# Kernel optimization log

Measured on AMD Instinct MI355X. Metric: run time of the kernel, lower is better.

The kernel has to match this reference:

```python
import jax, jax.numpy as jnp
import numpy as np

EPS_MASK = 1e-9   # module fills masked scores with eps, NOT -inf
LN_EPS = 1e-5

def _layer_norm(x, g, b):
    mu = jnp.mean(x, axis=-1, keepdims=True)
    var = jnp.mean(jnp.square(x - mu), axis=-1, keepdims=True)
    return (x - mu) * jax.lax.rsqrt(var + LN_EPS) * g + b

def _mha(q_in, k_in, v_in, wq, bq, wk, bk, wv, bv, wo, bo, mask, nhead):
    B, Sq, D = q_in.shape
    dk = D // nhead
    def proj(x, w, b):
        y = x @ w + b                                   # [B,S,D]
        return y.reshape(B, -1, nhead, dk).transpose(0, 2, 1, 3)  # [B,h,S,dk]
    q, k, v = proj(q_in, wq, bq), proj(k_in, wk, bk), proj(v_in, wv, bv)
    scores = jnp.einsum('bhqd,bhkd->bhqk', q, k) / np.sqrt(dk).astype(q.dtype)
    if mask is not None:
        scores = jnp.where(mask[:, None, :, :] == 0, jnp.asarray(EPS_MASK, scores.dtype), scores)
    p = jax.nn.softmax(scores, axis=-1)                 # dropout = identity (eval)
    x = jnp.einsum('bhqk,bhkd->bhqd', p, v)
    x = x.transpose(0, 2, 1, 3).reshape(B, Sq, D)
    return x @ wo + bo

def _forward_post(tgt, memory, tgt_pos, memory_pos, tgt_mask, memory_mask, p):
    nhead = 8
    # self-attention (q=k=tgt+pos, v=tgt)
    q = tgt + tgt_pos
    sa = _mha(q, q, tgt, p['sa_wq'], p['sa_bq'], p['sa_wk'], p['sa_bk'],
              p['sa_wv'], p['sa_bv'], p['sa_wo'], p['sa_bo'], tgt_mask, nhead)
    tgt = _layer_norm(tgt + sa, p['ln1_g'], p['ln1_b'])
    # cross-attention (q=tgt+tgt_pos, k=memory+memory_pos, v=memory)
    mq = tgt + tgt_pos
    mk = memory + memory_pos
    ca = _mha(mq, mk, memory, p['ca_wq'], p['ca_bq'], p['ca_wk'], p['ca_bk'],
              p['ca_wv'], p['ca_bv'], p['ca_wo'], p['ca_bo'], memory_mask, nhead)
    tgt = _layer_norm(tgt + ca, p['ln2_g'], p['ln2_b'])
    # FFN
    h = jax.nn.relu(tgt @ p['mlp_w1'] + p['mlp_b1'])
    ff = h @ p['mlp_w2'] + p['mlp_b2']
    return _layer_norm(tgt + ff, p['ln3_g'], p['ln3_b'])

def setup_inputs() -> dict:
    key = jax.random.key(0)
    B, S, M, D, H = 4, 1024, 1024, 512, 2048
    ks = iter(jax.random.split(key, 40))
    d = {
        'tgt': jax.random.normal(next(ks), (B, S, D), jnp.float32),
        'memory': jax.random.normal(next(ks), (B, M, D), jnp.float32),
        'tgt_pos': jax.random.normal(next(ks), (B, S, D), jnp.float32),
        'memory_pos': jax.random.normal(next(ks), (B, M, D), jnp.float32),
        'tgt_mask': jax.random.randint(next(ks), (B, S, S), 0, 2, jnp.int32),
        'memory_mask': jax.random.randint(next(ks), (B, S, M), 0, 2, jnp.int32),
    }
    for pre in ('sa', 'ca'):
        for nm in ('q', 'k', 'v', 'o'):
            d[f'{pre}_w{nm}'] = jax.random.normal(next(ks), (D, D), jnp.float32) * 0.02
            d[f'{pre}_b{nm}'] = jnp.zeros((D,), jnp.float32)
    for i in (1, 2, 3):
        d[f'ln{i}_g'] = jnp.ones((D,), jnp.float32)
        d[f'ln{i}_b'] = jnp.zeros((D,), jnp.float32)
    d['mlp_w1'] = jax.random.normal(next(ks), (D, H), jnp.float32) * 0.02
    d['mlp_b1'] = jnp.zeros((H,), jnp.float32)
    d['mlp_w2'] = jax.random.normal(next(ks), (H, D), jnp.float32) * 0.02
    d['mlp_b2'] = jnp.zeros((D,), jnp.float32)
    return d

def reference(tgt, memory, tgt_pos, memory_pos, tgt_mask, memory_mask,
              sa_wq, sa_bq, sa_wk, sa_bk, sa_wv, sa_bv, sa_wo, sa_bo,
              ca_wq, ca_bq, ca_wk, ca_bk, ca_wv, ca_bv, ca_wo, ca_bo,
              ln1_g, ln1_b, ln2_g, ln2_b, ln3_g, ln3_b,
              mlp_w1, mlp_b1, mlp_w2, mlp_b2):
    p = dict(sa_wq=sa_wq, sa_bq=sa_bq, sa_wk=sa_wk, sa_bk=sa_bk, sa_wv=sa_wv,
             sa_bv=sa_bv, sa_wo=sa_wo, sa_bo=sa_bo, ca_wq=ca_wq, ca_bq=ca_bq,
             ca_wk=ca_wk, ca_bk=ca_bk, ca_wv=ca_wv, ca_bv=ca_bv, ca_wo=ca_wo,
             ca_bo=ca_bo, ln1_g=ln1_g, ln1_b=ln1_b, ln2_g=ln2_g, ln2_b=ln2_b,
             ln3_g=ln3_g, ln3_b=ln3_b, mlp_w1=mlp_w1, mlp_b1=mlp_b1,
             mlp_w2=mlp_w2, mlp_b2=mlp_b2)
    return _forward_post(tgt, memory, tgt_pos, memory_pos, tgt_mask, memory_mask, p)
```

## Files before the change

kernel.cpp:

```cpp
#include <hip/hip_runtime.h>
#include <stdint.h>

typedef unsigned int u32;
typedef unsigned long long u64;
typedef unsigned short u16;
typedef __attribute__((ext_vector_type(8))) __bf16 bf16x8;
typedef __attribute__((ext_vector_type(4))) float f32x4;

#define DEV __device__ __forceinline__

DEV u16 f2bf(float f) {
    u32 x = __builtin_bit_cast(u32, f);
    u32 r = (x + 0x7FFFu + ((x >> 16) & 1u)) >> 16;
    return (u16)r;
}

DEV float bf2f(u16 x) {
    u32 u = (u32)x << 16;
    return __builtin_bit_cast(float, u);
}

DEV bf16x8 ldg8(const u16* p) {
    return __builtin_bit_cast(bf16x8, *(const uint4*)p);
}

DEV u32 pk2(float a, float b) {
    return (u32)f2bf(a) | ((u32)f2bf(b) << 16);
}

DEV void g2l16(const u16* g, u16* l) {
    __builtin_amdgcn_global_load_lds(
        (const __attribute__((address_space(1))) u32*)g,
        (__attribute__((address_space(3))) u32*)l, 16, 0, 0);
}

DEV f32x4 mfma16(bf16x8 a, bf16x8 b, f32x4 c) {
    return __builtin_amdgcn_mfma_f32_16x16x32_bf16(a, b, c, 0, 0, 0);
}

struct ProArgs {
    const float* w[10];
    u16* wtbase;
    const float4 *tgt, *tpos, *mem, *mpos;
    ushort4 *qin, *tgtb, *memb, *mkb;
    const int4 *m1, *m2;
    u32 *o1, *o2;
};
__global__ __launch_bounds__(256) void prologue_kernel(ProArgs a) {
    const int bx = blockIdx.x, t = threadIdx.x;
    if (bx < 10240) {
        int z = bx >> 10, bxx = bx & 1023;
        int Kd = (z == 9) ? 2048 : 512;
        int Nd = (z == 8) ? 2048 : 512;
        size_t off = (z < 8) ? (size_t)z * 262144
                             : (z == 8 ? (size_t)2097152 : (size_t)3145728);
        u16* out = a.wtbase + off;
        int nx = Nd / 32;
        int txile = bxx % nx, tyile = bxx / nx;
        if (tyile >= Kd / 32) return;
        const float* w = a.w[z];
        __shared__ float tl[32][33];
        int tx = t & 31, ty = t >> 5;
#pragma unroll
        for (int j = 0; j < 4; ++j)
            tl[ty + j * 8][tx] = w[(size_t)(tyile * 32 + ty + j * 8) * Nd + txile * 32 + tx];
        __syncthreads();
#pragma unroll
        for (int j = 0; j < 4; ++j)
            out[(size_t)(txile * 32 + ty + j * 8) * Kd + tyile * 32 + tx] = f2bf(tl[tx][ty + j * 8]);
    } else if (bx < 12288) {
        int i = (bx - 10240) * 256 + t;
        float4 tt = a.tgt[i], p = a.tpos[i], m = a.mem[i], mp = a.mpos[i];
        a.qin[i]  = make_ushort4(f2bf(tt.x + p.x), f2bf(tt.y + p.y), f2bf(tt.z + p.z), f2bf(tt.w + p.w));
        a.tgtb[i] = make_ushort4(f2bf(tt.x), f2bf(tt.y), f2bf(tt.z), f2bf(tt.w));
        a.memb[i] = make_ushort4(f2bf(m.x), f2bf(m.y), f2bf(m.z), f2bf(m.w));
        a.mkb[i]  = make_ushort4(f2bf(m.x + mp.x), f2bf(m.y + mp.y), f2bf(m.z + mp.z), f2bf(m.w + mp.w));
    } else {
        int i = (bx - 12288) * 256 + t;
        const int n8 = 524288;
        bool first = i < n8;
        int idx = first ? i : i - n8;
        const int4* src = first ? a.m1 : a.m2;
        int4 x = src[idx * 2], y = src[idx * 2 + 1];
        u32 by = (u32)(x.x != 0) | ((u32)(x.y != 0) << 1) | ((u32)(x.z != 0) << 2) |
                 ((u32)(x.w != 0) << 3) | ((u32)(y.x != 0) << 4) | ((u32)(y.y != 0) << 5) |
                 ((u32)(y.z != 0) << 6) | ((u32)(y.w != 0) << 7);
        u32 w = by | (__shfl_down(by, 1) << 8) | (__shfl_down(by, 2) << 16) |
                (__shfl_down(by, 3) << 24);
        if ((t & 3) == 0) (first ? a.o1 : a.o2)[idx >> 2] = w;
    }
}

struct GemmSet { const u16* A; const u16* W; const float* bias; void* out; float oscale; int epi; };
struct GemmArgs3 { GemmSet s[3]; };

template <int BM, int BN>
__global__ __launch_bounds__(256) void gemm_kernel(GemmArgs3 args, int M, int N, int Kd) {
    constexpr int MF = BM / 32, NF = BN / 32;
    const GemmSet gs = args.s[blockIdx.z];
    const u16* __restrict__ A = gs.A;
    const u16* __restrict__ W = gs.W;
    const int t = threadIdx.x;
    const int lane = t & 63;
    const int g = lane >> 4, r16 = lane & 15;
    const int wave = t >> 6;
    const int wm = wave >> 1, wn = wave & 1;
    const int nwg = gridDim.x * gridDim.y;
    const int fid = blockIdx.y * gridDim.x + blockIdx.x;
    const int qq = nwg >> 3;
    const int lid = (fid & 7) * qq + (fid >> 3);
    const int m0 = (lid / gridDim.x) * BM, n0 = (lid % gridDim.x) * BN;

    __shared__ __align__(16) u16 As[BM * 64];
    __shared__ __align__(16) u16 Bs[BN * 64];

    f32x4 acc[MF][NF];
#pragma unroll
    for (int m = 0; m < MF; ++m)
#pragma unroll
        for (int n = 0; n < NF; ++n) acc[m][n] = f32x4{0.f, 0.f, 0.f, 0.f};

    for (int kk = 0; kk < Kd; kk += 64) {
        __syncthreads();
#pragma unroll
        for (int i = 0; i < BM / 32; ++i) {
            int cid = t + i * 256, row = cid >> 3, c = cid & 7;
            g2l16(A + (size_t)(m0 + row) * Kd + kk + ((c ^ (row & 7)) << 3), &As[cid << 3]);
        }
#pragma unroll
        for (int i = 0; i < BN / 32; ++i) {
            int cid = t + i * 256, row = cid >> 3, c = cid & 7;
            g2l16(W + (size_t)(n0 + row) * Kd + kk + ((c ^ (row & 7)) << 3), &Bs[cid << 3]);
        }
        __syncthreads();
#pragma unroll
        for (int ks = 0; ks < 2; ++ks) {
            bf16x8 af[MF], bfr[NF];
#pragma unroll
            for (int m = 0; m < MF; ++m) {
                int row = wm * (MF * 16) + m * 16 + r16;
                af[m] = *(const bf16x8*)&As[(row << 6) + (((ks * 4 + g) ^ (row & 7)) << 3)];
            }
#pragma unroll
            for (int n = 0; n < NF; ++n) {
                int row = wn * (NF * 16) + n * 16 + r16;
                bfr[n] = *(const bf16x8*)&Bs[(row << 6) + (((ks * 4 + g) ^ (row & 7)) << 3)];
            }
#pragma unroll
            for (int m = 0; m < MF; ++m)
#pragma unroll
                for (int n = 0; n < NF; ++n)
                    acc[m][n] = mfma16(af[m], bfr[n], acc[m][n]);
        }
    }
    const int epi = gs.epi;
#pragma unroll
    for (int m = 0; m < MF; ++m) {
        int row0 = m0 + wm * (MF * 16) + m * 16 + g * 4;
#pragma unroll
        for (int n = 0; n < NF; ++n) {
            int col = n0 + wn * (NF * 16) + n * 16 + r16;
            float bv = gs.bias[col];
            float v[4];
#pragma unroll
            for (int r = 0; r < 4; ++r) v[r] = (acc[m][n][r] + bv) * gs.oscale;
            if (epi == 1) {
#pragma unroll
                for (int r = 0; r < 4; ++r) v[r] = fmaxf(v[r], 0.f);
            }
            if (epi == 3) {
                int bb = row0 >> 10, s = row0 & 1023;
                u16* o = (u16*)gs.out +
                         ((size_t)(bb * 8 + (col >> 6)) * 64 + (col & 63)) * 1024 + s;
                *(ushort4*)o = make_ushort4(f2bf(v[0]), f2bf(v[1]), f2bf(v[2]), f2bf(v[3]));
            } else {
                u16* o = (u16*)gs.out;
#pragma unroll
                for (int r = 0; r < 4; ++r) o[(size_t)(row0 + r) * N + col] = f2bf(v[r]);
            }
        }
    }
}

__global__ __launch_bounds__(512) void attn_part_kernel(
    const u16* __restrict__ Q, const u16* __restrict__ K,
    const u16* __restrict__ VT, const u32* __restrict__ mb,
    u16* __restrict__ OP, float2* __restrict__ ML, int Lq, int Lk) {
    const int t = threadIdx.x, lane = t & 63, wave = t >> 6;
    const int g = lane >> 4, r16 = lane & 15;
    const int h = blockIdx.y;
    const int b = blockIdx.z >> 1, p = blockIdx.z & 1;
    const int bh = b * 8 + h;
    const int q0 = blockIdx.x * 128 + wave * 16;
    const int kc0 = p * (Lk >> 1);
    const int NCH = (Lk >> 1) >> 5;

    __shared__ __align__(16) u16 Ks[2][32][64];
    __shared__ __align__(16) u16 Vs[2][64][32];
    __shared__ __align__(16) u16 Pl[8][16][40];

    const size_t qrow = (size_t)b * Lq + q0 + r16;
    const u16* qp = Q + qrow * 512 + h * 64 + g * 8;
    bf16x8 qb0 = ldg8(qp), qb1 = ldg8(qp + 32);
    const u32* mrow = mb + qrow * (Lk >> 5);

    const int sid = t & 255;
    const bool isK = t < 256;
    const int srow = sid >> 3, sc = sid & 7;
    const int vd = sid >> 2, vc = sid & 3;
    const u16* sg = isK
        ? K + (size_t)b * Lk * 512 + h * 64 + (size_t)srow * 512 + ((sc ^ (srow & 7)) << 3)
        : VT + ((size_t)bh * 64 + vd) * Lk + (vc << 3);
    u16* const sl = (isK ? &Ks[0][0][0] : &Vs[0][0][0]) + sid * 8;
    const size_t sstride = isK ? 512 : 1;

    f32x4 acc[4];
#pragma unroll
    for (int dt = 0; dt < 4; ++dt) acc[dt] = f32x4{0.f, 0.f, 0.f, 0.f};
    float mrun = -INFINITY, lrun = 0.f;
    const f32x4 zf = {0.f, 0.f, 0.f, 0.f};

    g2l16(sg + (size_t)kc0 * sstride, sl);
    __syncthreads();

    for (int c = 0; c < NCH; ++c) {
        const int buf = c & 1, nbuf = buf ^ 1;
        const int kc = kc0 + c * 32;
        if (c + 1 < NCH)
            g2l16(sg + (size_t)(kc + 32) * sstride, sl + nbuf * 2048);
        const u16* kb = &Ks[buf][0][0];
        const u16* vb = &Vs[buf][0][0];
        const int r1 = 16 + r16;
        bf16x8 k00 = *(const bf16x8*)(kb + r16 * 64 + ((g ^ (r16 & 7)) << 3));
        bf16x8 k01 = *(const bf16x8*)(kb + r16 * 64 + (((4 + g) ^ (r16 & 7)) << 3));
        bf16x8 k10 = *(const bf16x8*)(kb + r1 * 64 + ((g ^ (r16 & 7)) << 3));
        bf16x8 k11 = *(const bf16x8*)(kb + r1 * 64 + (((4 + g) ^ (r16 & 7)) << 3));
        __builtin_amdgcn_s_setprio(1);
        f32x4 s0 = mfma16(k00, qb0, zf); s0 = mfma16(k01, qb1, s0);
        f32x4 s1 = mfma16(k10, qb0, zf); s1 = mfma16(k11, qb1, s1);
        __builtin_amdgcn_s_setprio(0);

        u32 mw = mrow[kc >> 5];
        float sv[8];
#pragma unroll
        for (int r = 0; r < 4; ++r) {
            sv[r]     = ((mw >> (g * 4 + r)) & 1) ? s0[r] : 1e-9f;
            sv[4 + r] = ((mw >> (16 + g * 4 + r)) & 1) ? s1[r] : 1e-9f;
        }
        float tm = fmaxf(fmaxf(fmaxf(sv[0], sv[1]), fmaxf(sv[2], sv[3])),
                         fmaxf(fmaxf(sv[4], sv[5]), fmaxf(sv[6], sv[7])));
        tm = fmaxf(tm, __shfl_xor(tm, 16));
        tm = fmaxf(tm, __shfl_xor(tm, 32));
        if (!__all(tm <= mrun + 8.f)) {
            float mn = fmaxf(mrun, tm);
            float alpha = __expf(mrun - mn);
            mrun = mn;
            lrun *= alpha;
#pragma unroll
            for (int r = 0; r < 4; ++r) {
                float ar = __shfl(alpha, g * 4 + r);
#pragma unroll
                for (int dt = 0; dt < 4; ++dt) acc[dt][r] *= ar;
            }
        }
        float ts = 0.f;
#pragma unroll
        for (int j = 0; j < 8; ++j) { sv[j] = __expf(sv[j] - mrun); ts += sv[j]; }
        ts += __shfl_xor(ts, 16);
        ts += __shfl_xor(ts, 32);
        lrun += ts;

        uint2 u0; u0.x = pk2(sv[0], sv[1]); u0.y = pk2(sv[2], sv[3]);
        uint2 u1; u1.x = pk2(sv[4], sv[5]); u1.y = pk2(sv[6], sv[7]);
        *(uint2*)&Pl[wave][r16][g * 4] = u0;
        *(uint2*)&Pl[wave][r16][16 + g * 4] = u1;
        bf16x8 pf = *(const bf16x8*)&Pl[wave][r16][g * 8];
        __builtin_amdgcn_s_setprio(1);
#pragma unroll
        for (int dt = 0; dt < 4; ++dt) {
            bf16x8 vf = *(const bf16x8*)(vb + (dt * 16 + r16) * 32 + g * 8);
            acc[dt] = mfma16(pf, vf, acc[dt]);
        }
        __builtin_amdgcn_s_setprio(0);
        __syncthreads();
    }

    if (lane < 16)
        ML[(size_t)p * 32768 + (size_t)bh * 1024 + q0 + lane] = make_float2(mrun, lrun);
    const size_t obase = (size_t)p * 2097152 + ((size_t)bh * 1024 + q0) * 64;
#pragma unroll
    for (int dt = 0; dt < 4; ++dt)
#pragma unroll
        for (int r = 0; r < 4; ++r)
            OP[obase + (size_t)(g * 4 + r) * 64 + dt * 16 + r16] = f2bf(acc[dt][r]);
}

__global__ __launch_bounds__(256) void attn_combine_kernel(
    const u16* __restrict__ OP, const float2* __restrict__ ML, u16* __restrict__ O) {
    int idx = blockIdx.x * 256 + threadIdx.x;
    int row = idx >> 6, d = idx & 63;
    float2 ml0 = ML[row], ml1 = ML[32768 + row];
    float M = fmaxf(ml0.x, ml1.x);
    float w0 = __expf(ml0.x - M), w1 = __expf(ml1.x - M);
    float den = ml0.y * w0 + ml1.y * w1;
    float v = (bf2f(OP[idx]) * w0 + bf2f(OP[2097152 + idx]) * w1) / den;
    int bh = row >> 10, q = row & 1023;
    int b = bh >> 3, h = bh & 7;
    O[((size_t)(b * 1024 + q)) * 512 + h * 64 + d] = f2bf(v);
}

template <int MODE>
__global__ __launch_bounds__(256) void ln_kernel(
    const float* __restrict__ a, const u16* __restrict__ bsrc,
    const float* __restrict__ gam, const float* __restrict__ bet,
    const float* __restrict__ pos,
    float* __restrict__ yf, u16* __restrict__ yb, u16* __restrict__ qb) {
    const int lane = threadIdx.x & 63;
    const int row = blockIdx.x * 4 + (threadIdx.x >> 6);
    const size_t base = (size_t)row * 512 + lane * 8;
    float4 av0 = ((const float4*)(a + base))[0];
    float4 av1 = ((const float4*)(a + base))[1];
    uint4 bu = *(const uint4*)(bsrc + base);
    float x[8] = {av0.x + bf2f((u16)bu.x),        av0.y + bf2f((u16)(bu.x >> 16)),
                  av0.z + bf2f((u16)bu.y),        av0.w + bf2f((u16)(bu.y >> 16)),
                  av1.x + bf2f((u16)bu.z),        av1.y + bf2f((u16)(bu.z >> 16)),
                  av1.z + bf2f((u16)bu.w),        av1.w + bf2f((u16)(bu.w >> 16))};
    float s1 = 0.f, s2 = 0.f;
#pragma unroll
    for (int j = 0; j < 8; ++j) { s1 += x[j]; s2 += x[j] * x[j]; }
#pragma unroll
    for (int d = 1; d < 64; d <<= 1) { s1 += __shfl_xor(s1, d); s2 += __shfl_xor(s2, d); }
    float mean = s1 * (1.f / 512.f);
    float var = s2 * (1.f / 512.f) - mean * mean;
    float rs = rsqrtf(var + 1e-5f);
    float4 gv0 = ((const float4*)(gam + lane * 8))[0];
    float4 gv1 = ((const float4*)(gam + lane * 8))[1];
    float4 be0 = ((const float4*)(bet + lane * 8))[0];
    float4 be1 = ((const float4*)(bet + lane * 8))[1];
    float gg[8] = {gv0.x, gv0.y, gv0.z, gv0.w, gv1.x, gv1.y, gv1.z, gv1.w};
    float bb[8] = {be0.x, be0.y, be0.z, be0.w, be1.x, be1.y, be1.z, be1.w};
    float y[8];
#pragma unroll
    for (int j = 0; j < 8; ++j) y[j] = (x[j] - mean) * rs * gg[j] + bb[j];
    ((float4*)(yf + base))[0] = make_float4(y[0], y[1], y[2], y[3]);
    ((float4*)(yf + base))[1] = make_float4(y[4], y[5], y[6], y[7]);
    if (MODE == 1) {
        ((ushort4*)(yb + base))[0] = make_ushort4(f2bf(y[0]), f2bf(y[1]), f2bf(y[2]), f2bf(y[3]));
        ((ushort4*)(yb + base))[1] = make_ushort4(f2bf(y[4]), f2bf(y[5]), f2bf(y[6]), f2bf(y[7]));
    }
    if (MODE == 0) {
        float4 p0 = ((const float4*)(pos + base))[0];
        float4 p1 = ((const float4*)(pos + base))[1];
        ((ushort4*)(qb + base))[0] = make_ushort4(f2bf(y[0] + p0.x), f2bf(y[1] + p0.y),
                                                  f2bf(y[2] + p0.z), f2bf(y[3] + p0.w));
        ((ushort4*)(qb + base))[1] = make_ushort4(f2bf(y[4] + p1.x), f2bf(y[5] + p1.y),
                                                  f2bf(y[6] + p1.z), f2bf(y[7] + p1.w));
    }
}

extern "C" void kernel_launch(void* const* d_in, const int* in_sizes, int n_in,
                              void* d_out, int out_size, void* d_ws, size_t ws_size,
                              hipStream_t stream) {
    (void)in_sizes; (void)n_in; (void)out_size; (void)ws_size;
    const float* tgt      = (const float*)d_in[0];
    const float* memory   = (const float*)d_in[1];
    const float* tgt_pos  = (const float*)d_in[2];
    const float* mem_pos  = (const float*)d_in[3];
    const int*   tgt_mask = (const int*)d_in[4];
    const int*   mem_mask = (const int*)d_in[5];
    const float* sa_b[4] = {(const float*)d_in[7], (const float*)d_in[9],
                            (const float*)d_in[11], (const float*)d_in[13]};
    const float* ca_b[4] = {(const float*)d_in[15], (const float*)d_in[17],
                            (const float*)d_in[19], (const float*)d_in[21]};
    const float* ln1_g = (const float*)d_in[22]; const float* ln1_b = (const float*)d_in[23];
    const float* ln2_g = (const float*)d_in[24]; const float* ln2_b = (const float*)d_in[25];
    const float* ln3_g = (const float*)d_in[26]; const float* ln3_b = (const float*)d_in[27];
    const float* mlp_b1 = (const float*)d_in[29];
    const float* mlp_b2 = (const float*)d_in[31];

    const size_t MiB = 1024 * 1024;
    char* ws = (char*)d_ws;
    u16*  WT  = (u16*)(ws + 0);
    u32*  MBS = (u32*)(ws + 8 * MiB);
    u32*  MBC = (u32*)(ws + 8 * MiB + 512 * 1024);
    u16*  QIN = (u16*)(ws + 9 * MiB);
    u16*  TGTB= (u16*)(ws + 13 * MiB);
    u16*  MEMB= (u16*)(ws + 17 * MiB);
    u16*  MKB = (u16*)(ws + 21 * MiB);
    u16*  QM  = (u16*)(ws + 25 * MiB);
    u16*  KM  = (u16*)(ws + 29 * MiB);
    u16*  VTM = (u16*)(ws + 37 * MiB);
    u16*  ATNB= (u16*)(ws + 41 * MiB);
    u16*  PROJB = (u16*)(ws + 45 * MiB);
    float* X1F = (float*)(ws + 53 * MiB);
    u16*  MQB = (u16*)(ws + 65 * MiB);
    float* X2F = (float*)(ws + 69 * MiB);
    u16*  X2B = (u16*)(ws + 77 * MiB);
    u16*  FFH = (u16*)(ws + 9 * MiB);
    u16*  OPB = (u16*)(ws + 96 * MiB);
    float2* MLB = (float2*)(ws + 120 * MiB);

    u16* wt[10];
    for (int z = 0; z < 8; ++z) wt[z] = WT + (size_t)z * 262144;
    wt[8] = WT + 2097152;
    wt[9] = WT + 3145728;

    ProArgs pa;
    pa.w[0] = (const float*)d_in[6];  pa.w[1] = (const float*)d_in[8];
    pa.w[2] = (const float*)d_in[10]; pa.w[3] = (const float*)d_in[12];
    pa.w[4] = (const float*)d_in[14]; pa.w[5] = (const float*)d_in[16];
    pa.w[6] = (const float*)d_in[18]; pa.w[7] = (const float*)d_in[20];
    pa.w[8] = (const float*)d_in[28]; pa.w[9] = (const float*)d_in[30];
    pa.wtbase = WT;
    pa.tgt = (const float4*)tgt; pa.tpos = (const float4*)tgt_pos;
    pa.mem = (const float4*)memory; pa.mpos = (const float4*)mem_pos;
    pa.qin = (ushort4*)QIN; pa.tgtb = (ushort4*)TGTB;
    pa.memb = (ushort4*)MEMB; pa.mkb = (ushort4*)MKB;
    pa.m1 = (const int4*)tgt_mask; pa.m2 = (const int4*)mem_mask;
    pa.o1 = MBS; pa.o2 = MBC;
    prologue_kernel<<<16384, 256, 0, stream>>>(pa);

    GemmArgs3 ga;
    ga.s[0] = {QIN,  wt[0], sa_b[0], QM,  0.125f, 0};
    ga.s[1] = {QIN,  wt[1], sa_b[1], KM,  1.f,    0};
    ga.s[2] = {TGTB, wt[2], sa_b[2], VTM, 1.f,    3};
    gemm_kernel<128, 64><<<dim3(8, 32, 3), 256, 0, stream>>>(ga, 4096, 512, 512);
    attn_part_kernel<<<dim3(8, 8, 8), 512, 0, stream>>>(QM, KM, VTM, MBS, OPB, MLB, 1024, 1024);
    attn_combine_kernel<<<8192, 256, 0, stream>>>(OPB, MLB, ATNB);
    ga.s[0] = {ATNB, wt[3], sa_b[3], PROJB, 1.f, 0}; ga.s[1] = ga.s[0]; ga.s[2] = ga.s[0];
    gemm_kernel<64, 64><<<dim3(8, 64, 1), 256, 0, stream>>>(ga, 4096, 512, 512);
    ln_kernel<0><<<1024, 256, 0, stream>>>(tgt, PROJB, ln1_g, ln1_b, tgt_pos, X1F, nullptr, MQB);

    ga.s[0] = {MQB,  wt[4], ca_b[0], QM,  0.125f, 0};
    ga.s[1] = {MKB,  wt[5], ca_b[1], KM,  1.f,    0};
    ga.s[2] = {MEMB, wt[6], ca_b[2], VTM, 1.f,    3};
    gemm_kernel<128, 64><<<dim3(8, 32, 3), 256, 0, stream>>>(ga, 4096, 512, 512);
    attn_part_kernel<<<dim3(8, 8, 8), 512, 0, stream>>>(QM, KM, VTM, MBC, OPB, MLB, 1024, 1024);
    attn_combine_kernel<<<8192, 256, 0, stream>>>(OPB, MLB, ATNB);
    ga.s[0] = {ATNB, wt[7], ca_b[3], PROJB, 1.f, 0}; ga.s[1] = ga.s[0]; ga.s[2] = ga.s[0];
    gemm_kernel<64, 64><<<dim3(8, 64, 1), 256, 0, stream>>>(ga, 4096, 512, 512);
    ln_kernel<1><<<1024, 256, 0, stream>>>(X1F, PROJB, ln2_g, ln2_b, nullptr, X2F, X2B, nullptr);

    ga.s[0] = {X2B, wt[8], mlp_b1, FFH, 1.f, 1}; ga.s[1] = ga.s[0]; ga.s[2] = ga.s[0];
    gemm_kernel<128, 128><<<dim3(16, 32, 1), 256, 0, stream>>>(ga, 4096, 2048, 512);
    ga.s[0] = {FFH, wt[9], mlp_b2, PROJB, 1.f, 0}; ga.s[1] = ga.s[0]; ga.s[2] = ga.s[0];
    gemm_kernel<64, 64><<<dim3(8, 64, 1), 256, 0, stream>>>(ga, 4096, 512, 2048);
    ln_kernel<2><<<1024, 256, 0, stream>>>(X2F, PROJB, ln3_g, ln3_b, nullptr,
                                           (float*)d_out, nullptr, nullptr);
}
```

Measured before the change: 187.5 us.

## Hoist cross-attention K/V projections into self-attention QKV GEMM launch

The cross-attention K and V projections depend only on memory, so they are batched into the first grouped GEMM launch (5 z-slices instead of 3), leaving a single Q projection GEMM for cross-attention. This aims to fill the GPU better and shorten the serial chain, and separate workspace buffers are added for the two K/V pairs. Independently, the s_setprio hints around the MFMAs in the attention kernel are removed, and the FFN up-projection tile changes from 128x128 to 128x64 with twice as many blocks. The cross-attention Q-only GEMM now launches just 256 blocks, which may underutilise the device.

```diff
diff --git a/kernel.cpp b/kernel.cpp
--- a/kernel.cpp
+++ b/kernel.cpp
@@ -92,10 +92,10 @@
 }
 
 struct GemmSet { const u16* A; const u16* W; const float* bias; void* out; float oscale; int epi; };
-struct GemmArgs3 { GemmSet s[3]; };
+struct GemmArgs5 { GemmSet s[5]; };
 
 template <int BM, int BN>
-__global__ __launch_bounds__(256) void gemm_kernel(GemmArgs3 args, int M, int N, int Kd) {
+__global__ __launch_bounds__(256) void gemm_kernel(GemmArgs5 args, int M, int N, int Kd) {
     constexpr int MF = BM / 32, NF = BN / 32;
     const GemmSet gs = args.s[blockIdx.z];
     const u16* __restrict__ A = gs.A;
@@ -235,10 +235,8 @@
         bf16x8 k01 = *(const bf16x8*)(kb + r16 * 64 + (((4 + g) ^ (r16 & 7)) << 3));
         bf16x8 k10 = *(const bf16x8*)(kb + r1 * 64 + ((g ^ (r16 & 7)) << 3));
         bf16x8 k11 = *(const bf16x8*)(kb + r1 * 64 + (((4 + g) ^ (r16 & 7)) << 3));
-        __builtin_amdgcn_s_setprio(1);
         f32x4 s0 = mfma16(k00, qb0, zf); s0 = mfma16(k01, qb1, s0);
         f32x4 s1 = mfma16(k10, qb0, zf); s1 = mfma16(k11, qb1, s1);
-        __builtin_amdgcn_s_setprio(0);
 
         u32 mw = mrow[kc >> 5];
         float sv[8];
@@ -275,13 +273,11 @@
         *(uint2*)&Pl[wave][r16][g * 4] = u0;
         *(uint2*)&Pl[wave][r16][16 + g * 4] = u1;
         bf16x8 pf = *(const bf16x8*)&Pl[wave][r16][g * 8];
-        __builtin_amdgcn_s_setprio(1);
 #pragma unroll
         for (int dt = 0; dt < 4; ++dt) {
             bf16x8 vf = *(const bf16x8*)(vb + (dt * 16 + r16) * 32 + g * 8);
             acc[dt] = mfma16(pf, vf, acc[dt]);
         }
-        __builtin_amdgcn_s_setprio(0);
         __syncthreads();
     }
 
@@ -388,14 +384,16 @@
     u16*  MEMB= (u16*)(ws + 17 * MiB);
     u16*  MKB = (u16*)(ws + 21 * MiB);
     u16*  QM  = (u16*)(ws + 25 * MiB);
-    u16*  KM  = (u16*)(ws + 29 * MiB);
-    u16*  VTM = (u16*)(ws + 37 * MiB);
-    u16*  ATNB= (u16*)(ws + 41 * MiB);
-    u16*  PROJB = (u16*)(ws + 45 * MiB);
+    u16*  KMS = (u16*)(ws + 29 * MiB);
+    u16*  KMC = (u16*)(ws + 33 * MiB);
+    u16*  VTS = (u16*)(ws + 37 * MiB);
+    u16*  VTC = (u16*)(ws + 41 * MiB);
+    u16*  ATNB= (u16*)(ws + 45 * MiB);
+    u16*  PROJB = (u16*)(ws + 49 * MiB);
     float* X1F = (float*)(ws + 53 * MiB);
-    u16*  MQB = (u16*)(ws + 65 * MiB);
-    float* X2F = (float*)(ws + 69 * MiB);
-    u16*  X2B = (u16*)(ws + 77 * MiB);
+    u16*  MQB = (u16*)(ws + 61 * MiB);
+    float* X2F = (float*)(ws + 65 * MiB);
+    u16*  X2B = (u16*)(ws + 73 * MiB);
     u16*  FFH = (u16*)(ws + 9 * MiB);
     u16*  OPB = (u16*)(ws + 96 * MiB);
     float2* MLB = (float2*)(ws + 120 * MiB);
@@ -420,30 +418,35 @@
     pa.o1 = MBS; pa.o2 = MBC;
     prologue_kernel<<<16384, 256, 0, stream>>>(pa);
 
-    GemmArgs3 ga;
+    GemmArgs5 ga;
     ga.s[0] = {QIN,  wt[0], sa_b[0], QM,  0.125f, 0};
-    ga.s[1] = {QIN,  wt[1], sa_b[1], KM,  1.f,    0};
-    ga.s[2] = {TGTB, wt[2], sa_b[2], VTM, 1.f,    3};
-    gemm_kernel<128, 64><<<dim3(8, 32, 3), 256, 0, stream>>>(ga, 4096, 512, 512);
-    attn_part_kernel<<<dim3(8, 8, 8), 512, 0, stream>>>(QM, KM, VTM, MBS, OPB, MLB, 1024, 1024);
+    ga.s[1] = {QIN,  wt[1], sa_b[1], KMS, 1.f,    0};
+    ga.s[2] = {TGTB, wt[2], sa_b[2], VTS, 1.f,    3};
+    ga.s[3] = {MKB,  wt[5], ca_b[1], KMC, 1.f,    0};
+    ga.s[4] = {MEMB, wt[6], ca_b[2], VTC, 1.f,    3};
+    gemm_kernel<128, 64><<<dim3(8, 32, 5), 256, 0, stream>>>(ga, 4096, 512, 512);
+    attn_part_kernel<<<dim3(8, 8, 8), 512, 0, stream>>>(QM, KMS, VTS, MBS, OPB, MLB, 1024, 1024);
     attn_combine_kernel<<<8192, 256, 0, stream>>>(OPB, MLB, ATNB);
-    ga.s[0] = {ATNB, wt[3], sa_b[3], PROJB, 1.f, 0}; ga.s[1] = ga.s[0]; ga.s[2] = ga.s[0];
+    ga.s[0] = {ATNB, wt[3], sa_b[3], PROJB, 1.f, 0};
+    ga.s[1] = ga.s[0]; ga.s[2] = ga.s[0]; ga.s[3] = ga.s[0]; ga.s[4] = ga.s[0];
     gemm_kernel<64, 64><<<dim3(8, 64, 1), 256, 0, stream>>>(ga, 4096, 512, 512);
     ln_kernel<0><<<1024, 256, 0, stream>>>(tgt, PROJB, ln1_g, ln1_b, tgt_pos, X1F, nullptr, MQB);
 
-    ga.s[0] = {MQB,  wt[4], ca_b[0], QM,  0.125f, 0};
-    ga.s[1] = {MKB,  wt[5], ca_b[1], KM,  1.f,    0};
-    ga.s[2] = {MEMB, wt[6], ca_b[2], VTM, 1.f,    3};
-    gemm_kernel<128, 64><<<dim3(8, 32, 3), 256, 0, stream>>>(ga, 4096, 512, 512);
-    attn_part_kernel<<<dim3(8, 8, 8), 512, 0, stream>>>(QM, KM, VTM, MBC, OPB, MLB, 1024, 1024);
+    ga.s[0] = {MQB, wt[4], ca_b[0], QM, 0.125f, 0};
+    ga.s[1] = ga.s[0]; ga.s[2] = ga.s[0]; ga.s[3] = ga.s[0]; ga.s[4] = ga.s[0];
+    gemm_kernel<128, 64><<<dim3(8, 32, 1), 256, 0, stream>>>(ga, 4096, 512, 512);
+    attn_part_kernel<<<dim3(8, 8, 8), 512, 0, stream>>>(QM, KMC, VTC, MBC, OPB, MLB, 1024, 1024);
     attn_combine_kernel<<<8192, 256, 0, stream>>>(OPB, MLB, ATNB);
-    ga.s[0] = {ATNB, wt[7], ca_b[3], PROJB, 1.f, 0}; ga.s[1] = ga.s[0]; ga.s[2] = ga.s[0];
+    ga.s[0] = {ATNB, wt[7], ca_b[3], PROJB, 1.f, 0};
+    ga.s[1] = ga.s[0]; ga.s[2] = ga.s[0]; ga.s[3] = ga.s[0]; ga.s[4] = ga.s[0];
     gemm_kernel<64, 64><<<dim3(8, 64, 1), 256, 0, stream>>>(ga, 4096, 512, 512);
     ln_kernel<1><<<1024, 256, 0, stream>>>(X1F, PROJB, ln2_g, ln2_b, nullptr, X2F, X2B, nullptr);
 
-    ga.s[0] = {X2B, wt[8], mlp_b1, FFH, 1.f, 1}; ga.s[1] = ga.s[0]; ga.s[2] = ga.s[0];
-    gemm_kernel<128, 128><<<dim3(16, 32, 1), 256, 0, stream>>>(ga, 4096, 2048, 512);
-    ga.s[0] = {FFH, wt[9], mlp_b2, PROJB, 1.f, 0}; ga.s[1] = ga.s[0]; ga.s[2] = ga.s[0];
+    ga.s[0] = {X2B, wt[8], mlp_b1, FFH, 1.f, 1};
+    ga.s[1] = ga.s[0]; ga.s[2] = ga.s[0]; ga.s[3] = ga.s[0]; ga.s[4] = ga.s[0];
+    gemm_kernel<128, 64><<<dim3(32, 32, 1), 256, 0, stream>>>(ga, 4096, 2048, 512);
+    ga.s[0] = {FFH, wt[9], mlp_b2, PROJB, 1.f, 0};
+    ga.s[1] = ga.s[0]; ga.s[2] = ga.s[0]; ga.s[3] = ga.s[0]; ga.s[4] = ga.s[0];
     gemm_kernel<64, 64><<<dim3(8, 64, 1), 256, 0, stream>>>(ga, 4096, 512, 2048);
     ln_kernel<2><<<1024, 256, 0, stream>>>(X2F, PROJB, ln3_g, ln3_b, nullptr,
                                            (float*)d_out, nullptr, nullptr);
```

Result: no change. 184.5 us (-1.6%).
